# Performance work log

Hardware: AMD Instinct MI355X
Metric: run time of the kernel (lower is better)

## Reference

```python
import jax, jax.numpy as jnp
import numpy as np

SCALE = 4
KUP = 5


def conv2d(x, w, b, pad=0):
    # x: (B,C,H,W), w: (O,I,kh,kw)
    y = jax.lax.conv_general_dilated(x, w, (1, 1), [(pad, pad), (pad, pad)],
                                     dimension_numbers=('NCHW', 'OIHW', 'NCHW'))
    return y + b[None, :, None, None]


def unfold(x, k):
    # torch F.unfold equivalent: (B,C,H,W) -> (B,C,k*k,H,W), channel-major patch order
    p = jax.lax.conv_general_dilated_patches(x, (k, k), (1, 1), [(k // 2, k // 2), (k // 2, k // 2)])
    B, _, H, W = p.shape
    return p.reshape(B, -1, k * k, H, W)


def layernorm(x, g, b, eps=1e-5):
    m = jnp.mean(x, -1, keepdims=True)
    v = jnp.mean((x - m) ** 2, -1, keepdims=True)
    return (x - m) * jax.lax.rsqrt(v + eps) * g + b


def sim(q, k):
    # q: (B,sH,sW,E) high-res queries, k: (B,H,W,E) low-res keys
    B, H, W, C = k.shape
    s, ku = SCALE, KUP
    q6 = q.reshape(B, H, s, W, s, C)
    kunf = unfold(jnp.transpose(k, (0, 3, 1, 2)), ku)  # (B,E,ku^2,H,W)
    a = jnp.einsum('bhswtc,bcphw->bhswtp', q6, kunf)
    return a.reshape(B, s * H, s * W, ku * ku)


def atn(attn, x):
    # attn: (B,sH,sW,ku^2), x: (B,H,W,C) low-res values
    B, H, W, C = x.shape
    s, ku = SCALE, KUP
    a6 = attn.reshape(B, H, s, W, s, ku * ku)
    xunf = unfold(jnp.transpose(x, (0, 3, 1, 2)), ku)  # (B,C,ku^2,H,W)
    o = jnp.einsum('bhswtp,bcphw->bhswtc', a6, xunf)
    return o.reshape(B, s * H, s * W, C)


def setup_inputs() -> dict:
    key = jax.random.key(0)
    ks = jax.random.split(key, 40)
    B, C, H, W, yC, E = 2, 64, 128, 128, 3, 64
    sc = 0.05
    def n(i, shape):
        return jax.random.normal(ks[i], shape, jnp.float32) * sc
    return {
        'x': jax.random.normal(ks[0], (B, C, H, W), jnp.float32),
        'y': jax.random.normal(ks[1], (B, yC, H * SCALE, W * SCALE), jnp.float32),
        'gate_w': n(2, (C, C, 1, 1)), 'gate_b': n(3, (C,)),
        'pc1a_w': n(4, (16, yC + C, 1, 1)), 'pc1a_b': n(5, (16,)),
        'pc1b_w': n(6, (16, 16, 5, 5)), 'pc1b_b': n(7, (16,)),
        'spa1_w': n(8, (16, 16, 3, 3)), 'spa1_b': n(9, (16,)),
        'spa2_w': n(10, (16, 16, 3, 3)), 'spa2_b': n(11, (16,)),
        'frq1_w': n(12, (16, 16, 1, 1)), 'frq1_b': n(13, (16,)),
        'frq2_w': n(14, (16, 16, 1, 1)), 'frq2_b': n(15, (16,)),
        'cat_w': n(16, (8, 32, 1, 1)), 'cat_b': n(17, (8,)),
        'ca1_w': n(18, (2, 8, 1, 1)), 'ca1_b': n(19, (2,)),
        'ca2_w': n(20, (8, 2, 1, 1)), 'ca2_b': n(21, (8,)),
        'pc3_w': n(22, (C, 8, 1, 1)), 'pc3_b': n(23, (C,)),
        'lny_g': jnp.ones((C,), jnp.float32), 'lny_b': jnp.zeros((C,), jnp.float32),
        'lnx_g': jnp.ones((C,), jnp.float32), 'lnx_b': jnp.zeros((C,), jnp.float32),
        'q_w': n(24, (E, C)), 'q_b': n(25, (E,)),
        'k_w': n(26, (E, C)), 'k_b': n(27, (E,)),
    }


def reference(x, y, gate_w, gate_b, pc1a_w, pc1a_b, pc1b_w, pc1b_b,
              spa1_w, spa1_b, spa2_w, spa2_b, frq1_w, frq1_b, frq2_w, frq2_b,
              cat_w, cat_b, ca1_w, ca1_b, ca2_w, ca2_b, pc3_w, pc3_b,
              lny_g, lny_b, lnx_g, lnx_b, q_w, q_b, k_w, k_b):
    B, C, H, W = x.shape
    s = SCALE
    up_x = jax.image.resize(x, (B, C, H * s, W * s), 'cubic')
    gate = jax.nn.sigmoid(conv2d(up_x, gate_w, gate_b))
    # pan_conv1: 1x1 then 5x5
    f = conv2d(jnp.concatenate([y, up_x], 1), pc1a_w, pc1a_b)
    f = conv2d(f, pc1b_w, pc1b_b, pad=2)
    # DDNF: spatial branch (residual conv block stand-in) + frequency branch (1x1 stand-in), cat -> 8ch
    spa = f + conv2d(jax.nn.relu(conv2d(f, spa1_w, spa1_b, pad=1)), spa2_w, spa2_b, pad=1)
    frq = conv2d(jax.nn.relu(conv2d(f, frq1_w, frq1_b)), frq2_w, frq2_b)
    f = conv2d(jnp.concatenate([spa, frq], 1), cat_w, cat_b)
    # ChannelAttention(8, reduction=4): SE-style
    pooled = jnp.mean(f, (2, 3), keepdims=True)
    w = jax.nn.sigmoid(conv2d(jax.nn.relu(conv2d(pooled, ca1_w, ca1_b)), ca2_w, ca2_b))
    f = f * w
    enc = conv2d(f, pc3_w, pc3_b)  # (B,C,sH,sW)
    yb = jnp.transpose(enc, (0, 2, 3, 1))
    xb = jnp.transpose(x, (0, 2, 3, 1))
    yn = layernorm(yb, lny_g, lny_b)
    xn = layernorm(xb, lnx_g, lnx_b)
    q = yn @ q_w.T + q_b  # (B,sH,sW,E)
    k = xn @ k_w.T + k_b  # (B,H,W,E)
    attn = jax.nn.softmax(sim(q, k), axis=-1)
    sapa = jnp.transpose(atn(attn, xb), (0, 3, 1, 2))
    final = gate * sapa + (1.0 - gate) * enc
    return (final, sapa, enc)
```

## Files before the change

kernel.cpp:

```cpp
#include <hip/hip_runtime.h>
#include <hip/hip_bf16.h>
#include <math.h>


#define DEVFN static __device__ __forceinline__

DEVFN float keys_w(float d) {
    if (d < 1.f) return ((1.5f * d - 2.5f) * d) * d + 1.f;
    if (d < 2.f) return ((-0.5f * d + 2.5f) * d - 4.f) * d + 2.f;
    return 0.f;
}

DEVFN void bicubic_axis(int o, int n, int idx4[4], float w4[4]) {
    float f = (o + 0.5f) * 0.25f - 0.5f;
    float fb = floorf(f);
    int ib = (int)fb;
    float t = f - fb;
    float ws[4];
    ws[0] = keys_w(1.f + t);
    ws[1] = keys_w(t);
    ws[2] = keys_w(1.f - t);
    ws[3] = keys_w(2.f - t);
    float s = 0.f;
#pragma unroll
    for (int m = 0; m < 4; m++) {
        int ix = ib - 1 + m;
        if (ix < 0 || ix >= n) ws[m] = 0.f;
        s += ws[m];
        idx4[m] = min(max(ix, 0), n - 1);
    }
    float inv = 1.f / s;
#pragma unroll
    for (int m = 0; m < 4; m++) w4[m] = ws[m] * inv;
}

DEVFN float sigm(float v) { return 1.f / (1.f + __expf(-v)); }

DEVFN unsigned short f2bf(float f) {
    __hip_bfloat16 h = __float2bfloat16(f);
    unsigned short u;
    __builtin_memcpy(&u, &h, 2);
    return u;
}
DEVFN float bf2f(unsigned short u) {
    union { unsigned int i; float f; } z;
    z.i = ((unsigned int)u) << 16;
    return z.f;
}

__global__ __launch_bounds__(256) void k_prep(const float* __restrict__ w5,
                                              const float* __restrict__ w3a,
                                              const float* __restrict__ w3b,
                                              float* __restrict__ wT5,
                                              float* __restrict__ wT3a,
                                              float* __restrict__ wT3b) {
    int t = blockIdx.x * 256 + threadIdx.x;
    if (t < 6400) {
        int tap = t >> 8, ic = (t >> 4) & 15, oc = t & 15;
        wT5[t] = w5[(oc * 16 + ic) * 25 + tap];
    }
    if (t < 2304) {
        int tap = t >> 8, ic = (t >> 4) & 15, oc = t & 15;
        wT3a[t] = w3a[(oc * 16 + ic) * 9 + tap];
        wT3b[t] = w3b[(oc * 16 + ic) * 9 + tap];
    }
}

__global__ __launch_bounds__(256) void k_low(const float* __restrict__ x,
                                             const float* __restrict__ gw, const float* __restrict__ gb,
                                             const float* __restrict__ pw,
                                             const float* __restrict__ lg, const float* __restrict__ lb,
                                             const float* __restrict__ kw, const float* __restrict__ kbias,
                                             float* __restrict__ kb, float* __restrict__ xb,
                                             float* __restrict__ glo, float* __restrict__ plo) {
    int idx = blockIdx.x * 256 + threadIdx.x;
    int w = idx & 127, h = (idx >> 7) & 127, b = idx >> 14;
    const float* xp = x + (size_t)b * 64 * 16384 + (h << 7) + w;
    float xv[64];
#pragma unroll
    for (int c = 0; c < 64; c++) xv[c] = xp[(size_t)c << 14];
    float4* xbp = (float4*)(xb + (size_t)idx * 64);
#pragma unroll
    for (int c4 = 0; c4 < 16; c4++)
        xbp[c4] = make_float4(xv[4 * c4], xv[4 * c4 + 1], xv[4 * c4 + 2], xv[4 * c4 + 3]);
    float4* gp = (float4*)(glo + (size_t)idx * 64);
#pragma unroll
    for (int e4 = 0; e4 < 16; e4++) {
        float r[4];
#pragma unroll
        for (int u = 0; u < 4; u++) {
            int e = e4 * 4 + u;
            float s = gb[e];
#pragma unroll
            for (int c = 0; c < 64; c++) s = fmaf(xv[c], gw[e * 64 + c], s);
            r[u] = s;
        }
        gp[e4] = make_float4(r[0], r[1], r[2], r[3]);
    }
    float4* pp = (float4*)(plo + (size_t)idx * 16);
#pragma unroll
    for (int e4 = 0; e4 < 4; e4++) {
        float r[4];
#pragma unroll
        for (int u = 0; u < 4; u++) {
            int e = e4 * 4 + u;
            float s = 0.f;
#pragma unroll
            for (int c = 0; c < 64; c++) s = fmaf(xv[c], pw[e * 67 + 3 + c], s);
            r[u] = s;
        }
        pp[e4] = make_float4(r[0], r[1], r[2], r[3]);
    }
    float m = 0.f;
#pragma unroll
    for (int c = 0; c < 64; c++) m += xv[c];
    m *= (1.f / 64.f);
    float var = 0.f;
#pragma unroll
    for (int c = 0; c < 64; c++) {
        float d = xv[c] - m;
        var = fmaf(d, d, var);
    }
    var *= (1.f / 64.f);
    float rstd = rsqrtf(var + 1e-5f);
#pragma unroll
    for (int c = 0; c < 64; c++) xv[c] = (xv[c] - m) * rstd * lg[c] + lb[c];
    float4* kp = (float4*)(kb + (size_t)idx * 64);
#pragma unroll
    for (int e4 = 0; e4 < 16; e4++) {
        float r[4];
#pragma unroll
        for (int u = 0; u < 4; u++) {
            int e = e4 * 4 + u;
            float s = kbias[e];
#pragma unroll
            for (int c = 0; c < 64; c++) s = fmaf(xv[c], kw[e * 64 + c], s);
            r[u] = s;
        }
        kp[e4] = make_float4(r[0], r[1], r[2], r[3]);
    }
}

__global__ __launch_bounds__(256) void k_gp(const float* __restrict__ glo, const float* __restrict__ plo,
                                            const float* __restrict__ y,
                                            const float* __restrict__ paw, const float* __restrict__ pab,
                                            __hip_bfloat16* __restrict__ gate, float* __restrict__ f0) {
    __shared__ float v[68 * 81];
    int bid = blockIdx.x;
    int b = bid >> 10, i = (bid >> 1) & 511, j0 = (bid & 1) << 8;
    int t = threadIdx.x;
    int iy[4];
    float wy[4];
    bicubic_axis(i, 128, iy, wy);
    int c0 = (j0 >> 2) - 2;
    for (int e = t; e < 68 * 80; e += 256) {
        int ch = e % 80, lc = e / 80;
        int gc = c0 + lc;
        float val = 0.f;
        if ((unsigned)gc < 128u) {
            if (ch < 64) {
                val = wy[0] * glo[(size_t)((b * 128 + iy[0]) * 128 + gc) * 64 + ch] +
                      wy[1] * glo[(size_t)((b * 128 + iy[1]) * 128 + gc) * 64 + ch] +
                      wy[2] * glo[(size_t)((b * 128 + iy[2]) * 128 + gc) * 64 + ch] +
                      wy[3] * glo[(size_t)((b * 128 + iy[3]) * 128 + gc) * 64 + ch];
            } else {
                int cc = ch - 64;
                val = wy[0] * plo[(size_t)((b * 128 + iy[0]) * 128 + gc) * 16 + cc] +
                      wy[1] * plo[(size_t)((b * 128 + iy[1]) * 128 + gc) * 16 + cc] +
                      wy[2] * plo[(size_t)((b * 128 + iy[2]) * 128 + gc) * 16 + cc] +
                      wy[3] * plo[(size_t)((b * 128 + iy[3]) * 128 + gc) * 16 + cc];
            }
        }
        v[lc * 81 + ch] = val;
    }
    __syncthreads();
    int j = j0 + t;
    int jx[4];
    float wx[4];
    bicubic_axis(j, 128, jx, wx);
    int lx0 = jx[0] - c0, lx1 = jx[1] - c0, lx2 = jx[2] - c0, lx3 = jx[3] - c0;
    float out[80];
#pragma unroll
    for (int ch = 0; ch < 80; ch++)
        out[ch] = wx[0] * v[lx0 * 81 + ch] + wx[1] * v[lx1 * 81 + ch] +
                  wx[2] * v[lx2 * 81 + ch] + wx[3] * v[lx3 * 81 + ch];
    size_t pxoff = ((size_t)b << 18) + ((size_t)i << 9) + j;
    unsigned int uu[32];
#pragma unroll
    for (int k = 0; k < 32; k++) {
        unsigned short h0 = f2bf(sigm(out[2 * k]));
        unsigned short h1 = f2bf(sigm(out[2 * k + 1]));
        uu[k] = (unsigned int)h0 | ((unsigned int)h1 << 16);
    }
    uint4* gp4 = (uint4*)((unsigned short*)gate + pxoff * 64);
#pragma unroll
    for (int k4 = 0; k4 < 8; k4++)
        gp4[k4] = make_uint4(uu[4 * k4], uu[4 * k4 + 1], uu[4 * k4 + 2], uu[4 * k4 + 3]);
    float yc0 = y[((size_t)(b * 3 + 0) << 18) + ((size_t)i << 9) + j];
    float yc1 = y[((size_t)(b * 3 + 1) << 18) + ((size_t)i << 9) + j];
    float yc2 = y[((size_t)(b * 3 + 2) << 18) + ((size_t)i << 9) + j];
    float4* fp = (float4*)(f0 + pxoff * 16);
#pragma unroll
    for (int e4 = 0; e4 < 4; e4++) {
        float r[4];
#pragma unroll
        for (int u = 0; u < 4; u++) {
            int oc = e4 * 4 + u;
            r[u] = out[64 + oc] + pab[oc] + yc0 * paw[oc * 67 + 0] + yc1 * paw[oc * 67 + 1] + yc2 * paw[oc * 67 + 2];
        }
        fp[e4] = make_float4(r[0], r[1], r[2], r[3]);
    }
}

__global__ __launch_bounds__(256) void k_conv5(const float* __restrict__ fin,
                                               const float* __restrict__ wT,
                                               const float* __restrict__ bias,
                                               float* __restrict__ fout) {
    __shared__ float lds[8 * 68 * 20];
    int tid = threadIdx.x;
    int bid = blockIdx.x;
    int seg = bid & 7, it = (bid >> 3) & 127, b = bid >> 10;
    int i0 = it * 4, j0 = seg * 64;
    for (int s = tid; s < 2176; s += 256) {
        int part = s & 3, px = s >> 2;
        int row = px / 68, col = px - row * 68;
        int gi = i0 - 2 + row, gj = j0 - 2 + col;
        float4 v = make_float4(0.f, 0.f, 0.f, 0.f);
        if ((unsigned)gi < 512u && (unsigned)gj < 512u)
            v = *(const float4*)(fin + (((size_t)b << 18) + ((size_t)gi << 9) + gj) * 16 + part * 4);
        *(float4*)(&lds[(row * 68 + col) * 20 + part * 4]) = v;
    }
    __syncthreads();
    int tx = tid & 63, ty = tid >> 6;
    float acc[16];
#pragma unroll
    for (int oc = 0; oc < 16; oc++) acc[oc] = bias[oc];
#pragma unroll
    for (int ky = 0; ky < 5; ky++) {
#pragma unroll
        for (int kx = 0; kx < 5; kx++) {
            const float* p = &lds[((ty + ky) * 68 + tx + kx) * 20];
            float vv[16];
            *(float4*)(vv + 0) = *(const float4*)(p + 0);
            *(float4*)(vv + 4) = *(const float4*)(p + 4);
            *(float4*)(vv + 8) = *(const float4*)(p + 8);
            *(float4*)(vv + 12) = *(const float4*)(p + 12);
            const float* wp = wT + (ky * 5 + kx) * 256;
#pragma unroll
            for (int ic = 0; ic < 16; ic++) {
                float v = vv[ic];
#pragma unroll
                for (int oc = 0; oc < 16; oc++)
                    acc[oc] = fmaf(v, wp[ic * 16 + oc], acc[oc]);
            }
        }
    }
    int i = i0 + ty, j = j0 + tx;
    float4* op = (float4*)(fout + (((size_t)b << 18) + ((size_t)i << 9) + j) * 16);
    op[0] = make_float4(acc[0], acc[1], acc[2], acc[3]);
    op[1] = make_float4(acc[4], acc[5], acc[6], acc[7]);
    op[2] = make_float4(acc[8], acc[9], acc[10], acc[11]);
    op[3] = make_float4(acc[12], acc[13], acc[14], acc[15]);
}

__global__ __launch_bounds__(256) void k_conv3r(const float* __restrict__ fin,
                                                const float* __restrict__ wT,
                                                const float* __restrict__ bias,
                                                float* __restrict__ fout) {
    __shared__ float lds[6 * 66 * 20];
    int tid = threadIdx.x;
    int bid = blockIdx.x;
    int seg = bid & 7, it = (bid >> 3) & 127, b = bid >> 10;
    int i0 = it * 4, j0 = seg * 64;
    for (int s = tid; s < 1584; s += 256) {
        int part = s & 3, px = s >> 2;
        int row = px / 66, col = px - row * 66;
        int gi = i0 - 1 + row, gj = j0 - 1 + col;
        float4 v = make_float4(0.f, 0.f, 0.f, 0.f);
        if ((unsigned)gi < 512u && (unsigned)gj < 512u)
            v = *(const float4*)(fin + (((size_t)b << 18) + ((size_t)gi << 9) + gj) * 16 + part * 4);
        *(float4*)(&lds[(row * 66 + col) * 20 + part * 4]) = v;
    }
    __syncthreads();
    int tx = tid & 63, ty = tid >> 6;
    float acc[16];
#pragma unroll
    for (int oc = 0; oc < 16; oc++) acc[oc] = bias[oc];
#pragma unroll
    for (int ky = 0; ky < 3; ky++) {
#pragma unroll
        for (int kx = 0; kx < 3; kx++) {
            const float* p = &lds[((ty + ky) * 66 + tx + kx) * 20];
            float vv[16];
            *(float4*)(vv + 0) = *(const float4*)(p + 0);
            *(float4*)(vv + 4) = *(const float4*)(p + 4);
            *(float4*)(vv + 8) = *(const float4*)(p + 8);
            *(float4*)(vv + 12) = *(const float4*)(p + 12);
            const float* wp = wT + (ky * 3 + kx) * 256;
#pragma unroll
            for (int ic = 0; ic < 16; ic++) {
                float v = vv[ic];
#pragma unroll
                for (int oc = 0; oc < 16; oc++)
                    acc[oc] = fmaf(v, wp[ic * 16 + oc], acc[oc]);
            }
        }
    }
    int i = i0 + ty, j = j0 + tx;
    float4* op = (float4*)(fout + (((size_t)b << 18) + ((size_t)i << 9) + j) * 16);
    op[0] = make_float4(fmaxf(acc[0], 0.f), fmaxf(acc[1], 0.f), fmaxf(acc[2], 0.f), fmaxf(acc[3], 0.f));
    op[1] = make_float4(fmaxf(acc[4], 0.f), fmaxf(acc[5], 0.f), fmaxf(acc[6], 0.f), fmaxf(acc[7], 0.f));
    op[2] = make_float4(fmaxf(acc[8], 0.f), fmaxf(acc[9], 0.f), fmaxf(acc[10], 0.f), fmaxf(acc[11], 0.f));
    op[3] = make_float4(fmaxf(acc[12], 0.f), fmaxf(acc[13], 0.f), fmaxf(acc[14], 0.f), fmaxf(acc[15], 0.f));
}

__global__ __launch_bounds__(256) void k_tail(const float* __restrict__ f1,
                                              const float* __restrict__ t,
                                              const float* __restrict__ wT2,
                                              const float* __restrict__ s2b,
                                              const float* __restrict__ q1w, const float* __restrict__ q1b,
                                              const float* __restrict__ q2w, const float* __restrict__ q2b,
                                              const float* __restrict__ cw_, const float* __restrict__ cb_,
                                              float* __restrict__ f8) {
    __shared__ float lds[6 * 66 * 20];
    int tid = threadIdx.x;
    int bid = blockIdx.x;
    int seg = bid & 7, it = (bid >> 3) & 127, b = bid >> 10;
    int i0 = it * 4, j0 = seg * 64;
    for (int s = tid; s < 1584; s += 256) {
        int part = s & 3, px = s >> 2;
        int row = px / 66, col = px - row * 66;
        int gi = i0 - 1 + row, gj = j0 - 1 + col;
        float4 v = make_float4(0.f, 0.f, 0.f, 0.f);
        if ((unsigned)gi < 512u && (unsigned)gj < 512u)
            v = *(const float4*)(t + (((size_t)b << 18) + ((size_t)gi << 9) + gj) * 16 + part * 4);
        *(float4*)(&lds[(row * 66 + col) * 20 + part * 4]) = v;
    }
    __syncthreads();
    int tx = tid & 63, ty = tid >> 6;
    int i = i0 + ty, j = j0 + tx;
    float sp[16];
#pragma unroll
    for (int oc = 0; oc < 16; oc++) sp[oc] = s2b[oc];
#pragma unroll
    for (int ky = 0; ky < 3; ky++) {
#pragma unroll
        for (int kx = 0; kx < 3; kx++) {
            const float* p = &lds[((ty + ky) * 66 + tx + kx) * 20];
            float vv[16];
            *(float4*)(vv + 0) = *(const float4*)(p + 0);
            *(float4*)(vv + 4) = *(const float4*)(p + 4);
            *(float4*)(vv + 8) = *(const float4*)(p + 8);
            *(float4*)(vv + 12) = *(const float4*)(p + 12);
            const float* wp = wT2 + (ky * 3 + kx) * 256;
#pragma unroll
            for (int ic = 0; ic < 16; ic++) {
                float v = vv[ic];
#pragma unroll
                for (int oc = 0; oc < 16; oc++)
                    sp[oc] = fmaf(v, wp[ic * 16 + oc], sp[oc]);
            }
        }
    }
    float fv[16];
    const float4* f1p = (const float4*)(f1 + (((size_t)b << 18) + ((size_t)i << 9) + j) * 16);
    *(float4*)(fv + 0) = f1p[0];
    *(float4*)(fv + 4) = f1p[1];
    *(float4*)(fv + 8) = f1p[2];
    *(float4*)(fv + 12) = f1p[3];
#pragma unroll
    for (int c = 0; c < 16; c++) sp[c] += fv[c];
    float mid[16];
#pragma unroll
    for (int r = 0; r < 16; r++) {
        float m = q1b[r];
#pragma unroll
        for (int c = 0; c < 16; c++) m = fmaf(fv[c], q1w[r * 16 + c], m);
        mid[r] = fmaxf(m, 0.f);
    }
    float fo[16];
#pragma unroll
    for (int r = 0; r < 16; r++) {
        float m = q2b[r];
#pragma unroll
        for (int c = 0; c < 16; c++) m = fmaf(mid[c], q2w[r * 16 + c], m);
        fo[r] = m;
    }
    float r8[8];
#pragma unroll
    for (int o = 0; o < 8; o++) {
        float a = cb_[o];
#pragma unroll
        for (int c = 0; c < 16; c++) a = fmaf(sp[c], cw_[o * 32 + c], a);
#pragma unroll
        for (int c = 0; c < 16; c++) a = fmaf(fo[c], cw_[o * 32 + 16 + c], a);
        r8[o] = a;
    }
    float4* op = (float4*)(f8 + (((size_t)b << 18) + ((size_t)i << 9) + j) * 8);
    op[0] = make_float4(r8[0], r8[1], r8[2], r8[3]);
    op[1] = make_float4(r8[4], r8[5], r8[6], r8[7]);
}

__global__ __launch_bounds__(256) void k_pool(const float* __restrict__ f8, float* __restrict__ partials) {
    int b = blockIdx.x >> 4, blk = blockIdx.x & 15;
    const float4* fp = (const float4*)(f8 + (((size_t)b) << 18) * 8);
    float acc[8];
#pragma unroll
    for (int c = 0; c < 8; c++) acc[c] = 0.f;
    int p0 = blk * 16384;
    for (int p = p0 + threadIdx.x; p < p0 + 16384; p += 256) {
        float4 a0 = fp[p * 2], a1 = fp[p * 2 + 1];
        acc[0] += a0.x; acc[1] += a0.y; acc[2] += a0.z; acc[3] += a0.w;
        acc[4] += a1.x; acc[5] += a1.y; acc[6] += a1.z; acc[7] += a1.w;
    }
#pragma unroll
    for (int off = 32; off; off >>= 1) {
#pragma unroll
        for (int c = 0; c < 8; c++) acc[c] += __shfl_down(acc[c], off, 64);
    }
    __shared__ float ls[4][8];
    int lane = threadIdx.x & 63, wv = threadIdx.x >> 6;
    if (lane == 0) {
#pragma unroll
        for (int c = 0; c < 8; c++) ls[wv][c] = acc[c];
    }
    __syncthreads();
    if (threadIdx.x < 8) {
        float s = ls[0][threadIdx.x] + ls[1][threadIdx.x] + ls[2][threadIdx.x] + ls[3][threadIdx.x];
        partials[(b * 8 + threadIdx.x) * 16 + blk] = s;
    }
}

__global__ void k_se(const float* __restrict__ partials,
                     const float* __restrict__ w1, const float* __restrict__ b1,
                     const float* __restrict__ w2, const float* __restrict__ b2,
                     float* __restrict__ cw) {
    int b = threadIdx.x;
    if (b >= 2) return;
    float pooled[8];
#pragma unroll
    for (int c = 0; c < 8; c++) {
        float s = 0.f;
#pragma unroll
        for (int k = 0; k < 16; k++) s += partials[(b * 8 + c) * 16 + k];
        pooled[c] = s * (1.f / 262144.f);
    }
    float mid[2];
#pragma unroll
    for (int r = 0; r < 2; r++) {
        float m = b1[r];
#pragma unroll
        for (int c = 0; c < 8; c++) m = fmaf(w1[r * 8 + c], pooled[c], m);
        mid[r] = fmaxf(m, 0.f);
    }
#pragma unroll
    for (int c = 0; c < 8; c++) {
        float v = b2[c] + w2[c * 2 + 0] * mid[0] + w2[c * 2 + 1] * mid[1];
        cw[b * 8 + c] = 1.f / (1.f + __expf(-v));
    }
}

__global__ __launch_bounds__(256) void k_pc3(const float* __restrict__ f8, const float* __restrict__ cw,
                                             const float* __restrict__ w, const float* __restrict__ bias,
                                             const float* __restrict__ lg, const float* __restrict__ lb,
                                             const float* __restrict__ qw, const float* __restrict__ qbias,
                                             float* __restrict__ enc, unsigned short* __restrict__ qbuf) {
    int idx = blockIdx.x * 256 + threadIdx.x;
    int b = idx >> 18;
    size_t hi = (size_t)idx & 262143;
    const float4* fp = (const float4*)(f8 + (size_t)idx * 8);
    float4 a0 = fp[0], a1 = fp[1];
    float v[8] = {a0.x, a0.y, a0.z, a0.w, a1.x, a1.y, a1.z, a1.w};
#pragma unroll
    for (int c = 0; c < 8; c++) v[c] *= cw[b * 8 + c];
    float yn[64];
#pragma unroll
    for (int oc = 0; oc < 64; oc++) {
        float a = bias[oc];
#pragma unroll
        for (int c = 0; c < 8; c++) a = fmaf(v[c], w[oc * 8 + c], a);
        yn[oc] = a;
        enc[((size_t)(b * 64 + oc) << 18) + hi] = a;
    }
    float m = 0.f;
#pragma unroll
    for (int c = 0; c < 64; c++) m += yn[c];
    m *= (1.f / 64.f);
    float var = 0.f;
#pragma unroll
    for (int c = 0; c < 64; c++) {
        float d = yn[c] - m;
        var = fmaf(d, d, var);
    }
    var *= (1.f / 64.f);
    float rstd = rsqrtf(var + 1e-5f);
#pragma unroll
    for (int c = 0; c < 64; c++) yn[c] = (yn[c] - m) * rstd * lg[c] + lb[c];
    unsigned short* qp = qbuf + (size_t)idx * 64;
    for (int e0 = 0; e0 < 64; e0 += 8) {
        float qv[8];
#pragma unroll
        for (int u = 0; u < 8; u++) {
            float s = qbias[e0 + u];
#pragma unroll
            for (int c = 0; c < 64; c++) s = fmaf(yn[c], qw[(e0 + u) * 64 + c], s);
            qv[u] = s;
        }
        unsigned int pk[4];
#pragma unroll
        for (int u = 0; u < 4; u++)
            pk[u] = (unsigned int)f2bf(qv[2 * u]) | ((unsigned int)f2bf(qv[2 * u + 1]) << 16);
        *(uint4*)(qp + e0) = make_uint4(pk[0], pk[1], pk[2], pk[3]);
    }
}

__global__ __launch_bounds__(256, 4) void k_attn(const float* __restrict__ enc,
                                                 const __hip_bfloat16* __restrict__ gate,
                                                 const unsigned short* __restrict__ qb,
                                                 const float* __restrict__ kb, const float* __restrict__ xbv,
                                                 float* __restrict__ sapa, float* __restrict__ fin) {
    __shared__ float tile[100 * 68];
    int tid = threadIdx.x;
    int bid = blockIdx.x;
    int b = bid >> 12, i = (bid >> 3) & 511, jb = bid & 7;
    int j0 = jb << 6;
    int h = i >> 2;
    int wbase = j0 >> 2;
    int cg = tid & 3, px = tid >> 2;
    int j = j0 + px;
    size_t pix = ((size_t)b << 18) + ((size_t)i << 9) + j;
    const uint4* qp = (const uint4*)(qb + pix * 64 + cg * 16);
    uint4 q0 = qp[0], q1 = qp[1];
    unsigned int qu[8] = {q0.x, q0.y, q0.z, q0.w, q1.x, q1.y, q1.z, q1.w};
    float q[16];
#pragma unroll
    for (int k = 0; k < 8; k++) {
        q[2 * k] = bf2f((unsigned short)(qu[k] & 0xffff));
        q[2 * k + 1] = bf2f((unsigned short)(qu[k] >> 16));
    }
    for (int s = tid; s < 1600; s += 256) {
        int p = s >> 4, e4 = s & 15;
        int row = p / 20, col = p - row * 20;
        int hh = h - 2 + row, ww = wbase - 2 + col;
        float4 val = make_float4(0.f, 0.f, 0.f, 0.f);
        if ((unsigned)hh < 128u && (unsigned)ww < 128u)
            val = ((const float4*)(kb + (size_t)((b * 128 + hh) * 128 + ww) * 64))[e4];
        *(float4*)(tile + p * 68 + e4 * 4) = val;
    }
    __syncthreads();
    int wl = px >> 2;
    float a[25];
#pragma unroll
    for (int dy = 0; dy < 5; dy++) {
#pragma unroll
        for (int dx = 0; dx < 5; dx++) {
            int lp = dy * 20 + wl + dx;
            const float4* kp = (const float4*)(tile + lp * 68 + cg * 16);
            float s = 0.f;
#pragma unroll
            for (int e4 = 0; e4 < 4; e4++) {
                float4 kv = kp[e4];
                s = fmaf(q[4 * e4 + 0], kv.x, s);
                s = fmaf(q[4 * e4 + 1], kv.y, s);
                s = fmaf(q[4 * e4 + 2], kv.z, s);
                s = fmaf(q[4 * e4 + 3], kv.w, s);
            }
            a[dy * 5 + dx] = s;
        }
    }
#pragma unroll
    for (int p = 0; p < 25; p++) {
        a[p] += __shfl_xor(a[p], 1, 4);
        a[p] += __shfl_xor(a[p], 2, 4);
    }
    float mx = a[0];
#pragma unroll
    for (int p = 1; p < 25; p++) mx = fmaxf(mx, a[p]);
    float Z = 0.f;
#pragma unroll
    for (int p = 0; p < 25; p++) {
        a[p] = __expf(a[p] - mx);
        Z += a[p];
    }
    float invZ = 1.f / Z;
    __syncthreads();
    for (int s = tid; s < 1600; s += 256) {
        int p = s >> 4, e4 = s & 15;
        int row = p / 20, col = p - row * 20;
        int hh = h - 2 + row, ww = wbase - 2 + col;
        float4 val = make_float4(0.f, 0.f, 0.f, 0.f);
        if ((unsigned)hh < 128u && (unsigned)ww < 128u)
            val = ((const float4*)(xbv + (size_t)((b * 128 + hh) * 128 + ww) * 64))[e4];
        *(float4*)(tile + p * 68 + e4 * 4) = val;
    }
    __syncthreads();
    float o[16];
#pragma unroll
    for (int k = 0; k < 16; k++) o[k] = 0.f;
#pragma unroll
    for (int dy = 0; dy < 5; dy++) {
#pragma unroll
        for (int dx = 0; dx < 5; dx++) {
            float wp = a[dy * 5 + dx];
            int lp = dy * 20 + wl + dx;
            const float4* xp = (const float4*)(tile + lp * 68 + cg * 16);
#pragma unroll
            for (int e4 = 0; e4 < 4; e4++) {
                float4 xv = xp[e4];
                o[4 * e4 + 0] = fmaf(wp, xv.x, o[4 * e4 + 0]);
                o[4 * e4 + 1] = fmaf(wp, xv.y, o[4 * e4 + 1]);
                o[4 * e4 + 2] = fmaf(wp, xv.z, o[4 * e4 + 2]);
                o[4 * e4 + 3] = fmaf(wp, xv.w, o[4 * e4 + 3]);
            }
        }
    }
    const uint4* gp4 = (const uint4*)((const unsigned short*)gate + pix * 64 + cg * 16);
    uint4 g0 = gp4[0], g1 = gp4[1];
    unsigned int gu[8] = {g0.x, g0.y, g0.z, g0.w, g1.x, g1.y, g1.z, g1.w};
    size_t obase = ((size_t)b << 24) + ((size_t)i << 9) + j;
    const float* ep = enc + obase;
#pragma unroll
    for (int cc = 0; cc < 16; cc++) {
        int c = cg * 16 + cc;
        size_t oidx = obase + ((size_t)c << 18);
        float sv = o[cc] * invZ;
        __builtin_nontemporal_store(sv, &sapa[oidx]);
        unsigned int wbits = gu[cc >> 1];
        unsigned short hb = (cc & 1) ? (unsigned short)(wbits >> 16) : (unsigned short)(wbits & 0xffff);
        float gv = bf2f(hb);
        float ev = ep[(size_t)c << 18];
        __builtin_nontemporal_store(gv * sv + (1.f - gv) * ev, &fin[oidx]);
    }
}

extern "C" void kernel_launch(void* const* d_in, const int* in_sizes, int n_in,
                              void* d_out, int out_size, void* d_ws, size_t ws_size,
                              hipStream_t stream) {
    const float* x = (const float*)d_in[0];
    const float* y = (const float*)d_in[1];
    const float* gate_w = (const float*)d_in[2];
    const float* gate_b = (const float*)d_in[3];
    const float* pc1a_w = (const float*)d_in[4];
    const float* pc1a_b = (const float*)d_in[5];
    const float* pc1b_w = (const float*)d_in[6];
    const float* pc1b_b = (const float*)d_in[7];
    const float* spa1_w = (const float*)d_in[8];
    const float* spa1_b = (const float*)d_in[9];
    const float* spa2_w = (const float*)d_in[10];
    const float* spa2_b = (const float*)d_in[11];
    const float* frq1_w = (const float*)d_in[12];
    const float* frq1_b = (const float*)d_in[13];
    const float* frq2_w = (const float*)d_in[14];
    const float* frq2_b = (const float*)d_in[15];
    const float* cat_w = (const float*)d_in[16];
    const float* cat_b = (const float*)d_in[17];
    const float* ca1_w = (const float*)d_in[18];
    const float* ca1_b = (const float*)d_in[19];
    const float* ca2_w = (const float*)d_in[20];
    const float* ca2_b = (const float*)d_in[21];
    const float* pc3_w = (const float*)d_in[22];
    const float* pc3_b = (const float*)d_in[23];
    const float* lny_g = (const float*)d_in[24];
    const float* lny_b = (const float*)d_in[25];
    const float* lnx_g = (const float*)d_in[26];
    const float* lnx_b = (const float*)d_in[27];
    const float* q_w = (const float*)d_in[28];
    const float* q_b = (const float*)d_in[29];
    const float* k_w = (const float*)d_in[30];
    const float* k_b = (const float*)d_in[31];

    float* out = (float*)d_out;
    float* finalp = out;
    float* sapap = out + 33554432;
    float* encp = out + 67108864;

    char* ws = (char*)d_ws;
    __hip_bfloat16* gate = (__hip_bfloat16*)ws;
    float* f0 = (float*)(ws + 67108864);
    float* f1 = (float*)(ws + 100663296);
    float* f8 = (float*)(ws + 134217728);
    float* kbuf = (float*)(ws + 150994944);
    float* xbuf = (float*)(ws + 159383552);
    float* partials = (float*)(ws + 167772160);
    float* cw = (float*)(ws + 167773184);
    float* wT5 = (float*)(ws + 167773248);
    float* wT3a = (float*)(ws + 167798848);
    float* wT3b = (float*)(ws + 167808064);
    float* glo = f1;
    float* plo = f1 + 2097152;
    float* tbuf = f0;
    unsigned short* qbuf = (unsigned short*)(ws + 67108864);

    dim3 blk(256);
    dim3 gridHi(2048);
    dim3 gridConv(2048);

    k_prep<<<dim3(25), blk, 0, stream>>>(pc1b_w, spa1_w, spa2_w, wT5, wT3a, wT3b);
    k_low<<<dim3(128), blk, 0, stream>>>(x, gate_w, gate_b, pc1a_w, lnx_g, lnx_b, k_w, k_b,
                                         kbuf, xbuf, glo, plo);
    k_gp<<<gridHi, blk, 0, stream>>>(glo, plo, y, pc1a_w, pc1a_b, gate, f0);
    k_conv5<<<gridConv, blk, 0, stream>>>(f0, wT5, pc1b_b, f1);
    k_conv3r<<<gridConv, blk, 0, stream>>>(f1, wT3a, spa1_b, tbuf);
    k_tail<<<gridConv, blk, 0, stream>>>(f1, tbuf, wT3b, spa2_b, frq1_w, frq1_b,
                                         frq2_w, frq2_b, cat_w, cat_b, f8);
    k_pool<<<dim3(32), blk, 0, stream>>>(f8, partials);
    k_se<<<dim3(1), dim3(64), 0, stream>>>(partials, ca1_w, ca1_b, ca2_w, ca2_b, cw);
    k_pc3<<<gridHi, blk, 0, stream>>>(f8, cw, pc3_w, pc3_b, lny_g, lny_b, q_w, q_b, encp, qbuf);
    k_attn<<<dim3(8192), blk, 0, stream>>>(encp, gate, qbuf, kbuf, xbuf, sapap, finalp);
}
```

Baseline: 853.0 us.

## Store 16-channel intermediates in bf16 and recompute enc in attention kernel

Switches the high-resolution 16-channel intermediates (f0, f1, tbuf) from fp32 to bf16 storage, converting to fp32 on load, which halves their memory traffic. The attention kernel no longer reads enc back from the output buffer. It recomputes enc from the 8-channel f8 map, the SE weights and the pc3 1x1 weights. Nontemporal loads and stores are added for gate, q and enc. The cost is lower precision in the conv-chain intermediates and some extra FMAs in the attention epilogue.

```diff
diff --git a/kernel.cpp b/kernel.cpp
--- a/kernel.cpp
+++ b/kernel.cpp
@@ -4,6 +4,8 @@
 
 
 #define DEVFN static __device__ __forceinline__
+
+typedef unsigned int u32x4 __attribute__((ext_vector_type(4)));
 
 DEVFN float keys_w(float d) {
     if (d < 1.f) return ((1.5f * d - 2.5f) * d) * d + 1.f;
@@ -47,6 +49,10 @@
     z.i = ((unsigned int)u) << 16;
     return z.f;
 }
+DEVFN float4 cvt4(uint2 u) {
+    return make_float4(bf2f((unsigned short)(u.x & 0xffff)), bf2f((unsigned short)(u.x >> 16)),
+                       bf2f((unsigned short)(u.y & 0xffff)), bf2f((unsigned short)(u.y >> 16)));
+}
 
 __global__ __launch_bounds__(256) void k_prep(const float* __restrict__ w5,
                                               const float* __restrict__ w3a,
@@ -144,7 +150,7 @@
 __global__ __launch_bounds__(256) void k_gp(const float* __restrict__ glo, const float* __restrict__ plo,
                                             const float* __restrict__ y,
                                             const float* __restrict__ paw, const float* __restrict__ pab,
-                                            __hip_bfloat16* __restrict__ gate, float* __restrict__ f0) {
+                                            unsigned short* __restrict__ gate, unsigned short* __restrict__ f0) {
     __shared__ float v[68 * 81];
     int bid = blockIdx.x;
     int b = bid >> 10, i = (bid >> 1) & 511, j0 = (bid & 1) << 8;
@@ -185,37 +191,41 @@
         out[ch] = wx[0] * v[lx0 * 81 + ch] + wx[1] * v[lx1 * 81 + ch] +
                   wx[2] * v[lx2 * 81 + ch] + wx[3] * v[lx3 * 81 + ch];
     size_t pxoff = ((size_t)b << 18) + ((size_t)i << 9) + j;
-    unsigned int uu[32];
-#pragma unroll
-    for (int k = 0; k < 32; k++) {
-        unsigned short h0 = f2bf(sigm(out[2 * k]));
-        unsigned short h1 = f2bf(sigm(out[2 * k + 1]));
-        uu[k] = (unsigned int)h0 | ((unsigned int)h1 << 16);
-    }
-    uint4* gp4 = (uint4*)((unsigned short*)gate + pxoff * 64);
-#pragma unroll
-    for (int k4 = 0; k4 < 8; k4++)
-        gp4[k4] = make_uint4(uu[4 * k4], uu[4 * k4 + 1], uu[4 * k4 + 2], uu[4 * k4 + 3]);
+    u32x4* gp4 = (u32x4*)(gate + pxoff * 64);
+#pragma unroll
+    for (int k4 = 0; k4 < 8; k4++) {
+        u32x4 pk;
+#pragma unroll
+        for (int u = 0; u < 4; u++) {
+            int k = k4 * 4 + u;
+            pk[u] = (unsigned int)f2bf(sigm(out[2 * k])) | ((unsigned int)f2bf(sigm(out[2 * k + 1])) << 16);
+        }
+        __builtin_nontemporal_store(pk, gp4 + k4);
+    }
     float yc0 = y[((size_t)(b * 3 + 0) << 18) + ((size_t)i << 9) + j];
     float yc1 = y[((size_t)(b * 3 + 1) << 18) + ((size_t)i << 9) + j];
     float yc2 = y[((size_t)(b * 3 + 2) << 18) + ((size_t)i << 9) + j];
-    float4* fp = (float4*)(f0 + pxoff * 16);
-#pragma unroll
-    for (int e4 = 0; e4 < 4; e4++) {
-        float r[4];
+    float r[16];
+#pragma unroll
+    for (int oc = 0; oc < 16; oc++)
+        r[oc] = out[64 + oc] + pab[oc] + yc0 * paw[oc * 67 + 0] + yc1 * paw[oc * 67 + 1] + yc2 * paw[oc * 67 + 2];
+    uint4* fp = (uint4*)(f0 + pxoff * 16);
+#pragma unroll
+    for (int h4 = 0; h4 < 2; h4++) {
+        unsigned int pk[4];
 #pragma unroll
         for (int u = 0; u < 4; u++) {
-            int oc = e4 * 4 + u;
-            r[u] = out[64 + oc] + pab[oc] + yc0 * paw[oc * 67 + 0] + yc1 * paw[oc * 67 + 1] + yc2 * paw[oc * 67 + 2];
-        }
-        fp[e4] = make_float4(r[0], r[1], r[2], r[3]);
-    }
-}
-
-__global__ __launch_bounds__(256) void k_conv5(const float* __restrict__ fin,
+            int k = h4 * 4 + u;
+            pk[u] = (unsigned int)f2bf(r[2 * k]) | ((unsigned int)f2bf(r[2 * k + 1]) << 16);
+        }
+        fp[h4] = make_uint4(pk[0], pk[1], pk[2], pk[3]);
+    }
+}
+
+__global__ __launch_bounds__(256) void k_conv5(const unsigned short* __restrict__ fin,
                                                const float* __restrict__ wT,
                                                const float* __restrict__ bias,
-                                               float* __restrict__ fout) {
+                                               unsigned short* __restrict__ fout) {
     __shared__ float lds[8 * 68 * 20];
     int tid = threadIdx.x;
     int bid = blockIdx.x;
@@ -226,8 +236,10 @@
         int row = px / 68, col = px - row * 68;
         int gi = i0 - 2 + row, gj = j0 - 2 + col;
         float4 v = make_float4(0.f, 0.f, 0.f, 0.f);
-        if ((unsigned)gi < 512u && (unsigned)gj < 512u)
-            v = *(const float4*)(fin + (((size_t)b << 18) + ((size_t)gi << 9) + gj) * 16 + part * 4);
+        if ((unsigned)gi < 512u && (unsigned)gj < 512u) {
+            uint2 u = *(const uint2*)(fin + (((size_t)b << 18) + ((size_t)gi << 9) + gj) * 16 + part * 4);
+            v = cvt4(u);
+        }
         *(float4*)(&lds[(row * 68 + col) * 20 + part * 4]) = v;
     }
     __syncthreads();
@@ -256,17 +268,23 @@
         }
     }
     int i = i0 + ty, j = j0 + tx;
-    float4* op = (float4*)(fout + (((size_t)b << 18) + ((size_t)i << 9) + j) * 16);
-    op[0] = make_float4(acc[0], acc[1], acc[2], acc[3]);
-    op[1] = make_float4(acc[4], acc[5], acc[6], acc[7]);
-    op[2] = make_float4(acc[8], acc[9], acc[10], acc[11]);
-    op[3] = make_float4(acc[12], acc[13], acc[14], acc[15]);
-}
-
-__global__ __launch_bounds__(256) void k_conv3r(const float* __restrict__ fin,
+    uint4* op = (uint4*)(fout + (((size_t)b << 18) + ((size_t)i << 9) + j) * 16);
+#pragma unroll
+    for (int h4 = 0; h4 < 2; h4++) {
+        unsigned int pk[4];
+#pragma unroll
+        for (int u = 0; u < 4; u++) {
+            int k = h4 * 4 + u;
+            pk[u] = (unsigned int)f2bf(acc[2 * k]) | ((unsigned int)f2bf(acc[2 * k + 1]) << 16);
+        }
+        op[h4] = make_uint4(pk[0], pk[1], pk[2], pk[3]);
+    }
+}
+
+__global__ __launch_bounds__(256) void k_conv3r(const unsigned short* __restrict__ fin,
                                                 const float* __restrict__ wT,
                                                 const float* __restrict__ bias,
-                                                float* __restrict__ fout) {
+                                                unsigned short* __restrict__ fout) {
     __shared__ float lds[6 * 66 * 20];
     int tid = threadIdx.x;
     int bid = blockIdx.x;
@@ -277,8 +295,10 @@
         int row = px / 66, col = px - row * 66;
         int gi = i0 - 1 + row, gj = j0 - 1 + col;
         float4 v = make_float4(0.f, 0.f, 0.f, 0.f);
-        if ((unsigned)gi < 512u && (unsigned)gj < 512u)
-            v = *(const float4*)(fin + (((size_t)b << 18) + ((size_t)gi << 9) + gj) * 16 + part * 4);
+        if ((unsigned)gi < 512u && (unsigned)gj < 512u) {
+            uint2 u = *(const uint2*)(fin + (((size_t)b << 18) + ((size_t)gi << 9) + gj) * 16 + part * 4);
+            v = cvt4(u);
+        }
         *(float4*)(&lds[(row * 66 + col) * 20 + part * 4]) = v;
     }
     __syncthreads();
@@ -307,15 +327,22 @@
         }
     }
     int i = i0 + ty, j = j0 + tx;
-    float4* op = (float4*)(fout + (((size_t)b << 18) + ((size_t)i << 9) + j) * 16);
-    op[0] = make_float4(fmaxf(acc[0], 0.f), fmaxf(acc[1], 0.f), fmaxf(acc[2], 0.f), fmaxf(acc[3], 0.f));
-    op[1] = make_float4(fmaxf(acc[4], 0.f), fmaxf(acc[5], 0.f), fmaxf(acc[6], 0.f), fmaxf(acc[7], 0.f));
-    op[2] = make_float4(fmaxf(acc[8], 0.f), fmaxf(acc[9], 0.f), fmaxf(acc[10], 0.f), fmaxf(acc[11], 0.f));
-    op[3] = make_float4(fmaxf(acc[12], 0.f), fmaxf(acc[13], 0.f), fmaxf(acc[14], 0.f), fmaxf(acc[15], 0.f));
-}
-
-__global__ __launch_bounds__(256) void k_tail(const float* __restrict__ f1,
-                                              const float* __restrict__ t,
+    uint4* op = (uint4*)(fout + (((size_t)b << 18) + ((size_t)i << 9) + j) * 16);
+#pragma unroll
+    for (int h4 = 0; h4 < 2; h4++) {
+        unsigned int pk[4];
+#pragma unroll
+        for (int u = 0; u < 4; u++) {
+            int k = h4 * 4 + u;
+            pk[u] = (unsigned int)f2bf(fmaxf(acc[2 * k], 0.f)) |
+                    ((unsigned int)f2bf(fmaxf(acc[2 * k + 1], 0.f)) << 16);
+        }
+        op[h4] = make_uint4(pk[0], pk[1], pk[2], pk[3]);
+    }
+}
+
+__global__ __launch_bounds__(256) void k_tail(const unsigned short* __restrict__ f1,
+                                              const unsigned short* __restrict__ t,
                                               const float* __restrict__ wT2,
                                               const float* __restrict__ s2b,
                                               const float* __restrict__ q1w, const float* __restrict__ q1b,
@@ -332,8 +359,10 @@
         int row = px / 66, col = px - row * 66;
         int gi = i0 - 1 + row, gj = j0 - 1 + col;
         float4 v = make_float4(0.f, 0.f, 0.f, 0.f);
-        if ((unsigned)gi < 512u && (unsigned)gj < 512u)
-            v = *(const float4*)(t + (((size_t)b << 18) + ((size_t)gi << 9) + gj) * 16 + part * 4);
+        if ((unsigned)gi < 512u && (unsigned)gj < 512u) {
+            uint2 u = *(const uint2*)(t + (((size_t)b << 18) + ((size_t)gi << 9) + gj) * 16 + part * 4);
+            v = cvt4(u);
+        }
         *(float4*)(&lds[(row * 66 + col) * 20 + part * 4]) = v;
     }
     __syncthreads();
@@ -363,11 +392,14 @@
         }
     }
     float fv[16];
-    const float4* f1p = (const float4*)(f1 + (((size_t)b << 18) + ((size_t)i << 9) + j) * 16);
-    *(float4*)(fv + 0) = f1p[0];
-    *(float4*)(fv + 4) = f1p[1];
-    *(float4*)(fv + 8) = f1p[2];
-    *(float4*)(fv + 12) = f1p[3];
+    {
+        const uint2* f1p = (const uint2*)(f1 + (((size_t)b << 18) + ((size_t)i << 9) + j) * 16);
+#pragma unroll
+        for (int h4 = 0; h4 < 4; h4++) {
+            float4 v = cvt4(f1p[h4]);
+            fv[4 * h4 + 0] = v.x; fv[4 * h4 + 1] = v.y; fv[4 * h4 + 2] = v.z; fv[4 * h4 + 3] = v.w;
+        }
+    }
 #pragma unroll
     for (int c = 0; c < 16; c++) sp[c] += fv[c];
     float mid[16];
@@ -480,7 +512,7 @@
 #pragma unroll
         for (int c = 0; c < 8; c++) a = fmaf(v[c], w[oc * 8 + c], a);
         yn[oc] = a;
-        enc[((size_t)(b * 64 + oc) << 18) + hi] = a;
+        __builtin_nontemporal_store(a, &enc[((size_t)(b * 64 + oc) << 18) + hi]);
     }
     float m = 0.f;
 #pragma unroll
@@ -506,16 +538,17 @@
             for (int c = 0; c < 64; c++) s = fmaf(yn[c], qw[(e0 + u) * 64 + c], s);
             qv[u] = s;
         }
-        unsigned int pk[4];
+        u32x4 pk;
 #pragma unroll
         for (int u = 0; u < 4; u++)
             pk[u] = (unsigned int)f2bf(qv[2 * u]) | ((unsigned int)f2bf(qv[2 * u + 1]) << 16);
-        *(uint4*)(qp + e0) = make_uint4(pk[0], pk[1], pk[2], pk[3]);
-    }
-}
-
-__global__ __launch_bounds__(256, 4) void k_attn(const float* __restrict__ enc,
-                                                 const __hip_bfloat16* __restrict__ gate,
+        __builtin_nontemporal_store(pk, (u32x4*)(qp + e0));
+    }
+}
+
+__global__ __launch_bounds__(256, 4) void k_attn(const float* __restrict__ f8, const float* __restrict__ cwp,
+                                                 const float* __restrict__ pw, const float* __restrict__ pb,
+                                                 const unsigned short* __restrict__ gate,
                                                  const unsigned short* __restrict__ qb,
                                                  const float* __restrict__ kb, const float* __restrict__ xbv,
                                                  float* __restrict__ sapa, float* __restrict__ fin) {
@@ -529,9 +562,9 @@
     int cg = tid & 3, px = tid >> 2;
     int j = j0 + px;
     size_t pix = ((size_t)b << 18) + ((size_t)i << 9) + j;
-    const uint4* qp = (const uint4*)(qb + pix * 64 + cg * 16);
-    uint4 q0 = qp[0], q1 = qp[1];
-    unsigned int qu[8] = {q0.x, q0.y, q0.z, q0.w, q1.x, q1.y, q1.z, q1.w};
+    const u32x4* qp = (const u32x4*)(qb + pix * 64 + cg * 16);
+    u32x4 q0 = __builtin_nontemporal_load(qp), q1 = __builtin_nontemporal_load(qp + 1);
+    unsigned int qu[8] = {q0[0], q0[1], q0[2], q0[3], q1[0], q1[1], q1[2], q1[3]};
     float q[16];
 #pragma unroll
     for (int k = 0; k < 8; k++) {
@@ -614,21 +647,27 @@
             }
         }
     }
-    const uint4* gp4 = (const uint4*)((const unsigned short*)gate + pix * 64 + cg * 16);
-    uint4 g0 = gp4[0], g1 = gp4[1];
-    unsigned int gu[8] = {g0.x, g0.y, g0.z, g0.w, g1.x, g1.y, g1.z, g1.w};
+    const float4* fp8 = (const float4*)(f8 + pix * 8);
+    float4 a08 = fp8[0], a18 = fp8[1];
+    float v8[8] = {a08.x, a08.y, a08.z, a08.w, a18.x, a18.y, a18.z, a18.w};
+#pragma unroll
+    for (int c = 0; c < 8; c++) v8[c] *= cwp[b * 8 + c];
+    const u32x4* gp4 = (const u32x4*)(gate + pix * 64 + cg * 16);
+    u32x4 g0 = __builtin_nontemporal_load(gp4), g1 = __builtin_nontemporal_load(gp4 + 1);
+    unsigned int gu[8] = {g0[0], g0[1], g0[2], g0[3], g1[0], g1[1], g1[2], g1[3]};
     size_t obase = ((size_t)b << 24) + ((size_t)i << 9) + j;
-    const float* ep = enc + obase;
 #pragma unroll
     for (int cc = 0; cc < 16; cc++) {
         int c = cg * 16 + cc;
         size_t oidx = obase + ((size_t)c << 18);
         float sv = o[cc] * invZ;
         __builtin_nontemporal_store(sv, &sapa[oidx]);
+        float ev = pb[c];
+#pragma unroll
+        for (int u = 0; u < 8; u++) ev = fmaf(v8[u], pw[c * 8 + u], ev);
         unsigned int wbits = gu[cc >> 1];
         unsigned short hb = (cc & 1) ? (unsigned short)(wbits >> 16) : (unsigned short)(wbits & 0xffff);
         float gv = bf2f(hb);
-        float ev = ep[(size_t)c << 18];
         __builtin_nontemporal_store(gv * sv + (1.f - gv) * ev, &fin[oidx]);
     }
 }
@@ -675,9 +714,10 @@
     float* encp = out + 67108864;
 
     char* ws = (char*)d_ws;
-    __hip_bfloat16* gate = (__hip_bfloat16*)ws;
-    float* f0 = (float*)(ws + 67108864);
-    float* f1 = (float*)(ws + 100663296);
+    unsigned short* gate = (unsigned short*)ws;
+    unsigned short* f0 = (unsigned short*)(ws + 67108864);
+    unsigned short* f1 = (unsigned short*)(ws + 83886080);
+    unsigned short* tbuf = (unsigned short*)(ws + 100663296);
     float* f8 = (float*)(ws + 134217728);
     float* kbuf = (float*)(ws + 150994944);
     float* xbuf = (float*)(ws + 159383552);
@@ -686,9 +726,8 @@
     float* wT5 = (float*)(ws + 167773248);
     float* wT3a = (float*)(ws + 167798848);
     float* wT3b = (float*)(ws + 167808064);
-    float* glo = f1;
-    float* plo = f1 + 2097152;
-    float* tbuf = f0;
+    float* glo = (float*)(ws + 100663296);
+    float* plo = (float*)(ws + 109051904);
     unsigned short* qbuf = (unsigned short*)(ws + 67108864);
 
     dim3 blk(256);
@@ -706,5 +745,5 @@
     k_pool<<<dim3(32), blk, 0, stream>>>(f8, partials);
     k_se<<<dim3(1), dim3(64), 0, stream>>>(partials, ca1_w, ca1_b, ca2_w, ca2_b, cw);
     k_pc3<<<gridHi, blk, 0, stream>>>(f8, cw, pc3_w, pc3_b, lny_g, lny_b, q_w, q_b, encp, qbuf);
-    k_attn<<<dim3(8192), blk, 0, stream>>>(encp, gate, qbuf, kbuf, xbuf, sapap, finalp);
-}
+    k_attn<<<dim3(8192), blk, 0, stream>>>(f8, cw, pc3_w, pc3_b, gate, qbuf, kbuf, xbuf, sapap, finalp);
+}
```

Result: slower. 958.2 us (+12.3%).
